# Kernel tuning notes

Measured on AMD Instinct MI355X. Metric: run time of the kernel, lower is better.

The kernel has to match this reference:

```python
import jax, jax.numpy as jnp
import numpy as np

N_TOKENS = 32768
D_MODEL = 1024
NUM_CODES = 4096
CODE_DEPTH = 256


def setup_inputs() -> dict:
    key = jax.random.key(0)
    kx, kc, kw, kb = jax.random.split(key, 4)
    x = jax.random.normal(kx, (N_TOKENS, D_MODEL), dtype=jnp.float32)
    # codebook init mirrors the torch module: randn, row-normalized, first column zeroed
    cb = jax.random.normal(kc, (NUM_CODES, CODE_DEPTH), dtype=jnp.float32)
    cb = cb / jnp.linalg.norm(cb, axis=-1, keepdims=True)
    cb = cb.at[:, 0].set(0.0)
    W_down = jax.random.normal(kw, (D_MODEL, CODE_DEPTH), dtype=jnp.float32) * (D_MODEL ** -0.5)
    b_down = jax.random.normal(kb, (CODE_DEPTH,), dtype=jnp.float32) * 0.01
    return {"x": x, "codebook": cb, "W_down": W_down, "b_down": b_down}


def reference(x, codebook, W_down, b_down):
    # downsample d_model -> code_depth, then L2-normalize (eps=1e-6)
    z = x @ W_down + b_down                                   # [N, D]
    z = z / (jnp.linalg.norm(z, axis=-1, keepdims=True) + 1e-6)
    # squared euclidean distances to codebook[1:] (argmin of sq == argmin of cdist)
    cb = codebook[1:]                                         # [K-1, D]
    sq = (jnp.sum(z * z, axis=-1, keepdims=True)
          - 2.0 * (z @ cb.T)
          + jnp.sum(cb * cb, axis=-1))                        # [N, K-1]
    code_indices = jnp.argmin(sq, axis=-1) + 1                # [N], in [1, K)
    hard_codes = codebook[code_indices]                       # [N, D] gather
    return z, code_indices, hard_codes
```

## Files before the change

### kernel.cpp

```cpp
#include <hip/hip_runtime.h>
#include <math.h>
#include <stdint.h>

#define NT 32768
#define DM 1024
#define NC 4096
#define CD 256

#define X_F4 (DM/4)
#define W_F4 (CD/4)
#define Z_F4 (CD/4)
#define C_F4 (CD/4)

#define CDE 272
#define CDE_B (CDE*2)
#define TILE_B (32*CDE_B)

typedef __attribute__((ext_vector_type(8))) short bf16x8;
typedef __attribute__((ext_vector_type(4))) float floatx4;
typedef __attribute__((ext_vector_type(16))) float floatx16;

__device__ __forceinline__ unsigned short f2bf(float f) {
    union { float f; uint32_t u; } v; v.f = f;
    uint32_t u = v.u;
    u += 0x7FFFu + ((u >> 16) & 1u);
    return (unsigned short)(u >> 16);
}

__device__ __forceinline__ void split8(const float4 f0, const float4 f1,
                                       bf16x8& h, bf16x8& l) {
    float f[8] = {f0.x, f0.y, f0.z, f0.w, f1.x, f1.y, f1.z, f1.w};
    #pragma unroll
    for (int j = 0; j < 8; ++j) {
        union { float f; uint32_t u; } v; v.f = f[j];
        h[j] = (short)(v.u >> 16);
        union { uint32_t u; float f; } t; t.u = v.u & 0xFFFF0000u;
        l[j] = (short)f2bf(f[j] - t.f);
    }
}

__global__ __launch_bounds__(256) void k0_prep(const float4* __restrict__ cb,
                                               ushort* __restrict__ cbb2) {
    int wid = threadIdx.x >> 6, lane = threadIdx.x & 63;
    int code = blockIdx.x * 4 + wid;
    float4 c = cb[(size_t)code * C_F4 + lane];
    ushort4 h;
    h.x = f2bf(c.x); h.y = f2bf(c.y); h.z = f2bf(c.z); h.w = f2bf(c.w);
    *(ushort4*)(cbb2 + (size_t)code * CDE + lane * 4) = h;
    float ss = c.x*c.x + c.y*c.y + c.z*c.z + c.w*c.w;
    #pragma unroll
    for (int m = 32; m >= 1; m >>= 1) ss += __shfl_xor(ss, m, 64);
    if (lane == 0) {
        float nh = 2.0f - 0.5f * ss;
        union { float f; uint32_t u; } v; v.f = nh;
        uint32_t uh = v.u & 0xFFFF0000u;
        union { uint32_t u; float f; } t; t.u = uh;
        ushort* p = cbb2 + (size_t)code * CDE + 256;
        p[0] = (ushort)(uh >> 16);
        p[1] = f2bf(nh - t.f);
        #pragma unroll
        for (int i = 2; i < 16; ++i) p[i] = 0;
    }
}

__global__ __launch_bounds__(256) void k0b_wsplit(const float4* __restrict__ W,
                                                  ushort* __restrict__ WTh,
                                                  ushort* __restrict__ WTl) {
    __shared__ float lds[16][260];
    int slab = blockIdx.x;
    int tid = threadIdx.x;
    #pragma unroll
    for (int jj = 0; jj < 4; ++jj) {
        int v = jj * 256 + tid;
        int row = v >> 6, f4 = v & 63;
        float4 d = W[(size_t)(slab * 16 + row) * W_F4 + f4];
        *(float4*)&lds[row][f4 * 4] = d;
    }
    __syncthreads();
    int c = tid;
    #pragma unroll
    for (int kb = 0; kb < 2; ++kb) {
        bf16x8 h, l;
        #pragma unroll
        for (int j = 0; j < 8; ++j) {
            float x = lds[kb * 8 + j][c];
            union { float f; uint32_t u; } v; v.f = x;
            h[j] = (short)(v.u >> 16);
            union { uint32_t u; float f; } t; t.u = v.u & 0xFFFF0000u;
            l[j] = (short)f2bf(x - t.f);
        }
        size_t off = (size_t)c * 1024 + slab * 16 + kb * 8;
        *(bf16x8*)(WTh + off) = h;
        *(bf16x8*)(WTl + off) = l;
    }
}

__global__ __launch_bounds__(256, 2) void k1_gemm1(const float4* __restrict__ X,
                                                   const ushort* __restrict__ WTh,
                                                   const ushort* __restrict__ WTl,
                                                   float4* __restrict__ Zp) {
    __shared__ __align__(16) char lds[65536];
    char* Ah = lds;
    char* Al = lds + 16384;
    char* Bh = lds + 32768;
    char* Bl = lds + 49152;

    int tid  = threadIdx.x;
    int w    = tid >> 6, lane = tid & 63;
    int wm   = w >> 1, wn = w & 1;
    int c    = lane & 15, q = lane >> 4;
    int mb   = blockIdx.x >> 1, nb = blockIdx.x & 1;
    int m0   = mb * 128;
    int n0   = nb * 128;

    auto issue_loads = [&](int kt, float4* ga, bf16x8* gbh, bf16x8* gbl) {
        #pragma unroll
        for (int jj = 0; jj < 4; ++jj) {
            int v = jj * 256 + tid;
            int row = v >> 3, ch = v & 7;
            const float4* p = X + (size_t)(m0 + row) * X_F4 + kt * 16 + ch * 2;
            ga[jj * 2]     = p[0];
            ga[jj * 2 + 1] = p[1];
        }
        #pragma unroll
        for (int jj = 0; jj < 4; ++jj) {
            int v = jj * 256 + tid;
            int col = v >> 3, ch = v & 7;
            size_t off = (size_t)(n0 + col) * 1024 + kt * 64 + ch * 8;
            gbh[jj] = *(const bf16x8*)(WTh + off);
            gbl[jj] = *(const bf16x8*)(WTl + off);
        }
    };
    auto write_lds = [&](const float4* ga, const bf16x8* gbh, const bf16x8* gbl) {
        #pragma unroll
        for (int jj = 0; jj < 4; ++jj) {
            int v = jj * 256 + tid;
            int row = v >> 3, ch = v & 7;
            bf16x8 h, l;
            split8(ga[jj * 2], ga[jj * 2 + 1], h, l);
            int off = row * 128 + ((ch ^ (row & 7)) << 4);
            *(bf16x8*)(Ah + off) = h;
            *(bf16x8*)(Al + off) = l;
        }
        #pragma unroll
        for (int jj = 0; jj < 4; ++jj) {
            int v = jj * 256 + tid;
            int col = v >> 3, ch = v & 7;
            int off = col * 128 + ((ch ^ (col & 7)) << 4);
            *(bf16x8*)(Bh + off) = gbh[jj];
            *(bf16x8*)(Bl + off) = gbl[jj];
        }
    };

    floatx4 acc[4][4];
    #pragma unroll
    for (int i = 0; i < 4; ++i)
        #pragma unroll
        for (int j = 0; j < 4; ++j) acc[i][j] = (floatx4){0.f, 0.f, 0.f, 0.f};

    float4 ga[8]; bf16x8 gbh[4], gbl[4];
    issue_loads(0, ga, gbh, gbl);
    write_lds(ga, gbh, gbl);

    for (int kt = 0; kt < 16; ++kt) {
        __syncthreads();
        if (kt < 15) issue_loads(kt + 1, ga, gbh, gbl);

        #pragma unroll
        for (int ks = 0; ks < 2; ++ks) {
            bf16x8 xh[4], xl[4], wh[4], wl[4];
            #pragma unroll
            for (int i = 0; i < 4; ++i) {
                int xrow = wm * 64 + i * 16 + c;
                int xoff = xrow * 128 + (((ks * 4 + q) ^ (xrow & 7)) << 4);
                xh[i] = *(const bf16x8*)(Ah + xoff);
                xl[i] = *(const bf16x8*)(Al + xoff);
                int wrow = wn * 64 + i * 16 + c;
                int woff = wrow * 128 + (((ks * 4 + q) ^ (wrow & 7)) << 4);
                wh[i] = *(const bf16x8*)(Bh + woff);
                wl[i] = *(const bf16x8*)(Bl + woff);
            }
            #pragma unroll
            for (int xi = 0; xi < 4; ++xi)
                #pragma unroll
                for (int ni = 0; ni < 4; ++ni) {
                    acc[xi][ni] = __builtin_amdgcn_mfma_f32_16x16x32_bf16(wh[ni], xh[xi], acc[xi][ni], 0, 0, 0);
                    acc[xi][ni] = __builtin_amdgcn_mfma_f32_16x16x32_bf16(wh[ni], xl[xi], acc[xi][ni], 0, 0, 0);
                    acc[xi][ni] = __builtin_amdgcn_mfma_f32_16x16x32_bf16(wl[ni], xh[xi], acc[xi][ni], 0, 0, 0);
                }
        }

        __syncthreads();
        if (kt < 15) write_lds(ga, gbh, gbl);
    }

    #pragma unroll
    for (int xi = 0; xi < 4; ++xi) {
        int tok = m0 + wm * 64 + xi * 16 + c;
        #pragma unroll
        for (int ni = 0; ni < 4; ++ni) {
            int nf4 = nb * 32 + wn * 16 + ni * 4 + q;
            float4 o;
            o.x = acc[xi][ni][0]; o.y = acc[xi][ni][1];
            o.z = acc[xi][ni][2]; o.w = acc[xi][ni][3];
            Zp[(size_t)tok * Z_F4 + nf4] = o;
        }
    }
}

__global__ __launch_bounds__(256) void k1b_norm(float4* __restrict__ Z,
                                                const float4* __restrict__ bias) {
    int wid = threadIdx.x >> 6, lane = threadIdx.x & 63;
    int t = blockIdx.x * 4 + wid;
    float4 b = bias[lane];
    float4 z = Z[(size_t)t * Z_F4 + lane];
    z.x += b.x; z.y += b.y; z.z += b.z; z.w += b.w;
    double ss = (double)z.x*z.x + (double)z.y*z.y + (double)z.z*z.z + (double)z.w*z.w;
    #pragma unroll
    for (int m = 32; m >= 1; m >>= 1) ss += __shfl_xor(ss, m, 64);
    float inv = 1.0f / ((float)sqrt(ss) + 1e-6f);
    z.x *= inv; z.y *= inv; z.z *= inv; z.w *= inv;
    Z[(size_t)t * Z_F4 + lane] = z;
}

__global__ __launch_bounds__(256, 1) void k2_mfma(const float* __restrict__ Z,
                                                  const ushort* __restrict__ Cbb2,
                                                  int4* __restrict__ cands) {
    __shared__ uint32_t Mk[128][2][4];

    int tid  = threadIdx.x;
    int wm   = tid >> 6;
    int lane = tid & 63;
    int r    = lane & 31;
    int hi   = lane >> 5;
    int t0   = blockIdx.x * 128;

    bf16x8 Bt[17];
    #pragma unroll
    for (int f = 0; f < 16; ++f) {
        const float* zp = Z + (size_t)(t0 + wm * 32 + r) * CD + f * 16 + hi * 8;
        float4 f0 = *(const float4*)zp;
        float4 f1 = *(const float4*)(zp + 4);
        bf16x8 b;
        b[0] = (short)f2bf(f0.x); b[1] = (short)f2bf(f0.y);
        b[2] = (short)f2bf(f0.z); b[3] = (short)f2bf(f0.w);
        b[4] = (short)f2bf(f1.x); b[5] = (short)f2bf(f1.y);
        b[6] = (short)f2bf(f1.z); b[7] = (short)f2bf(f1.w);
        Bt[f] = b;
    }
    {
        bf16x8 b = (bf16x8){0, 0, 0, 0, 0, 0, 0, 0};
        if (hi == 0) { b[0] = (short)0x3F80; b[1] = (short)0x3F80; }
        Bt[16] = b;
    }

    int r0 = (r == 0) ? 1 : r;
    const char* abase   = (const char*)Cbb2;
    const char* ap_lane = abase + r * CDE_B + hi * 16;
    const char* ap0     = abase + r0 * CDE_B + hi * 16;

    uint32_t K1v = 0, K2v = 0, K3v = 0, K4v = 0;

    bf16x8 A0[17], A1[17];
    #pragma unroll
    for (int f = 0; f < 17; ++f) A0[f] = *(const bf16x8*)(ap0 + f * 32);

    const char* ap = ap_lane + TILE_B;

    auto compute = [&](const bf16x8 (&Ax)[17], int ct) {
        floatx16 Cc;
        #pragma unroll
        for (int i = 0; i < 16; ++i) Cc[i] = 0.0f;
        #pragma unroll
        for (int f = 0; f < 17; ++f)
            Cc = __builtin_amdgcn_mfma_f32_32x32x16_bf16(Ax[f], Bt[f], Cc, 0, 0, 0);
        #pragma unroll
        for (int reg = 0; reg < 16; ++reg) {
            union { float f; uint32_t u; } uv; uv.f = Cc[reg];
            uint32_t k = (uv.u & 0xFFFFF800u) | ((uint32_t)ct << 4) | (uint32_t)reg;
            uint32_t t;
            t = k < K1v ? k : K1v;  K1v = k > K1v ? k : K1v;  k = t;
            t = k < K2v ? k : K2v;  K2v = k > K2v ? k : K2v;  k = t;
            t = k < K3v ? k : K3v;  K3v = k > K3v ? k : K3v;  k = t;
            K4v = k > K4v ? k : K4v;
        }
    };

    for (int ct = 0; ct < 128; ct += 2) {
        #pragma unroll
        for (int f = 0; f < 17; ++f) A1[f] = *(const bf16x8*)(ap + f * 32);
        ap += TILE_B;
        compute(A0, ct);
        const char* apn = (ct + 2 < 128) ? ap : ap_lane;
        #pragma unroll
        for (int f = 0; f < 17; ++f) A0[f] = *(const bf16x8*)(apn + f * 32);
        ap += TILE_B;
        compute(A1, ct + 1);
        if ((ct & 15) == 14) __builtin_amdgcn_s_barrier();
    }

    int lt = wm * 32 + r;
    Mk[lt][hi][0] = K1v; Mk[lt][hi][1] = K2v;
    Mk[lt][hi][2] = K3v; Mk[lt][hi][3] = K4v;
    __syncthreads();

    if (tid < 128) {
        uint32_t bk0 = 0, bk1 = 0, bk2 = 0, bk3 = 0;
        uint32_t be0 = 0, be1 = 0, be2 = 0, be3 = 0;
        #pragma unroll
        for (int e = 0; e < 8; ++e) {
            uint32_t key = Mk[tid][e >> 2][e & 3];
            if (key > bk0) {
                bk3 = bk2; be3 = be2; bk2 = bk1; be2 = be1;
                bk1 = bk0; be1 = be0; bk0 = key; be0 = (uint32_t)e;
            } else if (key > bk1) {
                bk3 = bk2; be3 = be2; bk2 = bk1; be2 = be1; bk1 = key; be1 = (uint32_t)e;
            } else if (key > bk2) {
                bk3 = bk2; be3 = be2; bk2 = key; be2 = (uint32_t)e;
            } else if (key > bk3) {
                bk3 = key; be3 = (uint32_t)e;
            }
        }
        auto dec = [&](uint32_t key, uint32_t e) -> int {
            int ct = (int)((key >> 4) & 127u);
            int rg = (int)(key & 15u);
            int row = (rg & 3) + 8 * (rg >> 2) + 4 * (int)(e >> 2);
            int code = ct * 32 + row;
            return code < 1 ? 1 : code;
        };
        int4 out;
        out.x = dec(bk0, be0); out.y = dec(bk1, be1);
        out.z = dec(bk2, be2); out.w = dec(bk3, be3);
        cands[t0 + tid] = out;
    }
}

__global__ __launch_bounds__(256) void k3_refine(const float4* __restrict__ Z,
                                                 const float4* __restrict__ Cb,
                                                 const int4* __restrict__ cands,
                                                 float* __restrict__ idxOut,
                                                 float4* __restrict__ hardOut) {
    int wid = threadIdx.x >> 6, lane = threadIdx.x & 63;
    int t = blockIdx.x * 4 + wid;
    int4 cd = cands[t];
    int cc[4] = {cd.x, cd.y, cd.z, cd.w};
    float4 z = Z[(size_t)t * Z_F4 + lane];
    double best = -1.0e300;
    int bi = NC;
    #pragma unroll
    for (int e = 0; e < 4; ++e) {
        int idx = cc[e];
        float4 cf = Cb[(size_t)idx * C_F4 + lane];
        double dot = (double)z.x*cf.x + (double)z.y*cf.y + (double)z.z*cf.z + (double)z.w*cf.w;
        double nrm = (double)cf.x*cf.x + (double)cf.y*cf.y + (double)cf.z*cf.z + (double)cf.w*cf.w;
        #pragma unroll
        for (int m = 32; m >= 1; m >>= 1) {
            dot += __shfl_xor(dot, m, 64);
            nrm += __shfl_xor(nrm, m, 64);
        }
        double s = dot - 0.5 * nrm;
        if (idx >= 1 && (s > best || (s == best && idx < bi))) { best = s; bi = idx; }
    }
    if (lane == 0) idxOut[t] = (float)bi;
    hardOut[(size_t)t * C_F4 + lane] = Cb[(size_t)bi * C_F4 + lane];
}

extern "C" void kernel_launch(void* const* d_in, const int* in_sizes, int n_in,
                              void* d_out, int out_size, void* d_ws, size_t ws_size,
                              hipStream_t stream) {
    const float* x  = (const float*)d_in[0];
    const float* cb = (const float*)d_in[1];
    const float* w  = (const float*)d_in[2];
    const float* bd = (const float*)d_in[3];

    float* zOut    = (float*)d_out;
    float* idxOut  = zOut + (size_t)NT * CD;
    float* hardOut = idxOut + NT;

    int4*   cands = (int4*)d_ws;
    ushort* cbb2  = (ushort*)((char*)d_ws + 524288);
    ushort* wth   = (ushort*)((char*)d_ws + 2752512);
    ushort* wtl   = (ushort*)((char*)d_ws + 3276800);

    k0_prep<<<NC / 4, 256, 0, stream>>>((const float4*)cb, cbb2);
    k0b_wsplit<<<DM / 16, 256, 0, stream>>>((const float4*)w, wth, wtl);
    k1_gemm1<<<(NT / 128) * 2, 256, 0, stream>>>((const float4*)x, wth, wtl,
                                                 (float4*)zOut);
    k1b_norm<<<NT / 4, 256, 0, stream>>>((float4*)zOut, (const float4*)bd);
    k2_mfma<<<NT / 128, 256, 0, stream>>>(zOut, cbb2, cands);
    k3_refine<<<NT / 4, 256, 0, stream>>>((const float4*)zOut, (const float4*)cb,
                                          cands, idxOut, (float4*)hardOut);
}
```

Measured before the change: 441.0 us.

## Tile codebook into MFMA-fragment layout and split codes across waves

```diff
diff --git a/kernel.cpp b/kernel.cpp
--- a/kernel.cpp
+++ b/kernel.cpp
@@ -12,9 +12,7 @@
 #define Z_F4 (CD/4)
 #define C_F4 (CD/4)
 
-#define CDE 272
-#define CDE_B (CDE*2)
-#define TILE_B (32*CDE_B)
+#define TILE_B 17408
 
 typedef __attribute__((ext_vector_type(8))) short bf16x8;
 typedef __attribute__((ext_vector_type(4))) float floatx4;
@@ -41,25 +39,36 @@
 
 __global__ __launch_bounds__(256) void k0_prep(const float4* __restrict__ cb,
                                                ushort* __restrict__ cbb2) {
-    int wid = threadIdx.x >> 6, lane = threadIdx.x & 63;
-    int code = blockIdx.x * 4 + wid;
-    float4 c = cb[(size_t)code * C_F4 + lane];
-    ushort4 h;
-    h.x = f2bf(c.x); h.y = f2bf(c.y); h.z = f2bf(c.z); h.w = f2bf(c.w);
-    *(ushort4*)(cbb2 + (size_t)code * CDE + lane * 4) = h;
-    float ss = c.x*c.x + c.y*c.y + c.z*c.z + c.w*c.w;
-    #pragma unroll
-    for (int m = 32; m >= 1; m >>= 1) ss += __shfl_xor(ss, m, 64);
-    if (lane == 0) {
+    int tid = threadIdx.x;
+    int l = tid & 63, wid = tid >> 6;
+    int code = blockIdx.x * 8 + wid * 2 + (l >> 5);
+    int fr = l & 31, f = fr >> 1, hi = fr & 1;
+    const float4* p = cb + (size_t)code * C_F4 + f * 4 + hi * 2;
+    float4 f0 = p[0], f1 = p[1];
+    bf16x8 h;
+    h[0] = (short)f2bf(f0.x); h[1] = (short)f2bf(f0.y);
+    h[2] = (short)f2bf(f0.z); h[3] = (short)f2bf(f0.w);
+    h[4] = (short)f2bf(f1.x); h[5] = (short)f2bf(f1.y);
+    h[6] = (short)f2bf(f1.z); h[7] = (short)f2bf(f1.w);
+    float ss = f0.x*f0.x + f0.y*f0.y + f0.z*f0.z + f0.w*f0.w
+             + f1.x*f1.x + f1.y*f1.y + f1.z*f1.z + f1.w*f1.w;
+    #pragma unroll
+    for (int m = 16; m >= 1; m >>= 1) ss += __shfl_xor(ss, m, 64);
+    int ct = code >> 5, r = code & 31;
+    char* base = (char*)cbb2 + (size_t)ct * TILE_B;
+    *(bf16x8*)(base + f * 1024 + (((hi << 5) | r) << 4)) = h;
+    if (fr == 0) {
         float nh = 2.0f - 0.5f * ss;
         union { float f; uint32_t u; } v; v.f = nh;
         uint32_t uh = v.u & 0xFFFF0000u;
         union { uint32_t u; float f; } t; t.u = uh;
-        ushort* p = cbb2 + (size_t)code * CDE + 256;
-        p[0] = (ushort)(uh >> 16);
-        p[1] = f2bf(nh - t.f);
-        #pragma unroll
-        for (int i = 2; i < 16; ++i) p[i] = 0;
+        bf16x8 e = (bf16x8){0, 0, 0, 0, 0, 0, 0, 0};
+        e[0] = (short)(uh >> 16);
+        e[1] = (short)f2bf(nh - t.f);
+        *(bf16x8*)(base + 16 * 1024 + (r << 4)) = e;
+    } else if (fr == 1) {
+        bf16x8 z = (bf16x8){0, 0, 0, 0, 0, 0, 0, 0};
+        *(bf16x8*)(base + 16 * 1024 + ((32 | r) << 4)) = z;
     }
 }
 
@@ -223,17 +232,19 @@
     Z[(size_t)t * Z_F4 + lane] = z;
 }
 
-__global__ __launch_bounds__(256, 1) void k2_mfma(const float* __restrict__ Z,
+__global__ __launch_bounds__(256, 2) void k2_mfma(const float* __restrict__ Z,
                                                   const ushort* __restrict__ Cbb2,
                                                   int4* __restrict__ cands) {
-    __shared__ uint32_t Mk[128][2][4];
+    __shared__ uint32_t Mk[64][4][4];
 
     int tid  = threadIdx.x;
-    int wm   = tid >> 6;
+    int w    = tid >> 6;
+    int wm   = w >> 1;
+    int wc   = w & 1;
     int lane = tid & 63;
     int r    = lane & 31;
     int hi   = lane >> 5;
-    int t0   = blockIdx.x * 128;
+    int t0   = blockIdx.x * 64;
 
     bf16x8 Bt[17];
     #pragma unroll
@@ -254,18 +265,18 @@
         Bt[16] = b;
     }
 
-    int r0 = (r == 0) ? 1 : r;
-    const char* abase   = (const char*)Cbb2;
-    const char* ap_lane = abase + r * CDE_B + hi * 16;
-    const char* ap0     = abase + r0 * CDE_B + hi * 16;
-
-    uint32_t K1v = 0, K2v = 0, K3v = 0, K4v = 0;
+    const char* half = (const char*)Cbb2 + (size_t)(wc * 64) * TILE_B;
+    int l0 = (wc == 0 && r == 0) ? (lane + 1) : lane;
+    const char* ap0 = half + l0 * 16;
+    const char* apL = half + lane * 16;
+
+    float K1f = 0.0f, K2f = 0.0f, K3f = 0.0f, K4f = 0.0f;
 
     bf16x8 A0[17], A1[17];
     #pragma unroll
-    for (int f = 0; f < 17; ++f) A0[f] = *(const bf16x8*)(ap0 + f * 32);
-
-    const char* ap = ap_lane + TILE_B;
+    for (int f = 0; f < 17; ++f) A0[f] = *(const bf16x8*)(ap0 + f * 1024);
+
+    const char* ap = apL + TILE_B;
 
     auto compute = [&](const bf16x8 (&Ax)[17], int ct) {
         floatx16 Cc;
@@ -277,54 +288,63 @@
         #pragma unroll
         for (int reg = 0; reg < 16; ++reg) {
             union { float f; uint32_t u; } uv; uv.f = Cc[reg];
-            uint32_t k = (uv.u & 0xFFFFF800u) | ((uint32_t)ct << 4) | (uint32_t)reg;
-            uint32_t t;
-            t = k < K1v ? k : K1v;  K1v = k > K1v ? k : K1v;  k = t;
-            t = k < K2v ? k : K2v;  K2v = k > K2v ? k : K2v;  k = t;
-            t = k < K3v ? k : K3v;  K3v = k > K3v ? k : K3v;  k = t;
-            K4v = k > K4v ? k : K4v;
+            uint32_t ku = (uv.u & 0xFFFFF800u) | ((uint32_t)ct << 4) | (uint32_t)reg;
+            union { uint32_t u; float f; } kv; kv.u = ku;
+            float k = kv.f;
+            K4f = __builtin_amdgcn_fmed3f(K3f, K4f, k);
+            K3f = __builtin_amdgcn_fmed3f(K2f, K3f, k);
+            K2f = __builtin_amdgcn_fmed3f(K1f, K2f, k);
+            K1f = fmaxf(K1f, k);
         }
     };
 
-    for (int ct = 0; ct < 128; ct += 2) {
-        #pragma unroll
-        for (int f = 0; f < 17; ++f) A1[f] = *(const bf16x8*)(ap + f * 32);
+    for (int ctl = 0; ctl < 64; ctl += 2) {
+        #pragma unroll
+        for (int f = 0; f < 17; ++f) A1[f] = *(const bf16x8*)(ap + f * 1024);
         ap += TILE_B;
-        compute(A0, ct);
-        const char* apn = (ct + 2 < 128) ? ap : ap_lane;
-        #pragma unroll
-        for (int f = 0; f < 17; ++f) A0[f] = *(const bf16x8*)(apn + f * 32);
+        compute(A0, wc * 64 + ctl);
+        const char* apn = (ctl + 2 < 64) ? ap : apL;
+        #pragma unroll
+        for (int f = 0; f < 17; ++f) A0[f] = *(const bf16x8*)(apn + f * 1024);
         ap += TILE_B;
-        compute(A1, ct + 1);
-        if ((ct & 15) == 14) __builtin_amdgcn_s_barrier();
-    }
-
-    int lt = wm * 32 + r;
-    Mk[lt][hi][0] = K1v; Mk[lt][hi][1] = K2v;
-    Mk[lt][hi][2] = K3v; Mk[lt][hi][3] = K4v;
+        compute(A1, wc * 64 + ctl + 1);
+        if ((ctl & 15) == 14) __builtin_amdgcn_s_barrier();
+    }
+
+    {
+        int lt = wm * 32 + r, src = wc * 2 + hi;
+        union { float f; uint32_t u; } a, b, c, d;
+        a.f = K1f; b.f = K2f; c.f = K3f; d.f = K4f;
+        Mk[lt][src][0] = a.u; Mk[lt][src][1] = b.u;
+        Mk[lt][src][2] = c.u; Mk[lt][src][3] = d.u;
+    }
     __syncthreads();
 
-    if (tid < 128) {
+    if (tid < 64) {
         uint32_t bk0 = 0, bk1 = 0, bk2 = 0, bk3 = 0;
         uint32_t be0 = 0, be1 = 0, be2 = 0, be3 = 0;
         #pragma unroll
-        for (int e = 0; e < 8; ++e) {
-            uint32_t key = Mk[tid][e >> 2][e & 3];
-            if (key > bk0) {
-                bk3 = bk2; be3 = be2; bk2 = bk1; be2 = be1;
-                bk1 = bk0; be1 = be0; bk0 = key; be0 = (uint32_t)e;
-            } else if (key > bk1) {
-                bk3 = bk2; be3 = be2; bk2 = bk1; be2 = be1; bk1 = key; be1 = (uint32_t)e;
-            } else if (key > bk2) {
-                bk3 = bk2; be3 = be2; bk2 = key; be2 = (uint32_t)e;
-            } else if (key > bk3) {
-                bk3 = key; be3 = (uint32_t)e;
+        for (int s = 0; s < 4; ++s) {
+            #pragma unroll
+            for (int j = 0; j < 4; ++j) {
+                uint32_t key = Mk[tid][s][j];
+                uint32_t e = (uint32_t)s;
+                if (key > bk0) {
+                    bk3 = bk2; be3 = be2; bk2 = bk1; be2 = be1;
+                    bk1 = bk0; be1 = be0; bk0 = key; be0 = e;
+                } else if (key > bk1) {
+                    bk3 = bk2; be3 = be2; bk2 = bk1; be2 = be1; bk1 = key; be1 = e;
+                } else if (key > bk2) {
+                    bk3 = bk2; be3 = be2; bk2 = key; be2 = e;
+                } else if (key > bk3) {
+                    bk3 = key; be3 = e;
+                }
             }
         }
         auto dec = [&](uint32_t key, uint32_t e) -> int {
             int ct = (int)((key >> 4) & 127u);
             int rg = (int)(key & 15u);
-            int row = (rg & 3) + 8 * (rg >> 2) + 4 * (int)(e >> 2);
+            int row = (rg & 3) + 8 * (rg >> 2) + 4 * (int)(e & 1);
             int code = ct * 32 + row;
             return code < 1 ? 1 : code;
         };
@@ -382,12 +402,12 @@
     ushort* wth   = (ushort*)((char*)d_ws + 2752512);
     ushort* wtl   = (ushort*)((char*)d_ws + 3276800);
 
-    k0_prep<<<NC / 4, 256, 0, stream>>>((const float4*)cb, cbb2);
+    k0_prep<<<NC / 8, 256, 0, stream>>>((const float4*)cb, cbb2);
     k0b_wsplit<<<DM / 16, 256, 0, stream>>>((const float4*)w, wth, wtl);
     k1_gemm1<<<(NT / 128) * 2, 256, 0, stream>>>((const float4*)x, wth, wtl,
                                                  (float4*)zOut);
     k1b_norm<<<NT / 4, 256, 0, stream>>>((float4*)zOut, (const float4*)bd);
-    k2_mfma<<<NT / 128, 256, 0, stream>>>(zOut, cbb2, cands);
+    k2_mfma<<<NT / 64, 256, 0, stream>>>(zOut, cbb2, cands);
     k3_refine<<<NT / 4, 256, 0, stream>>>((const float4*)zOut, (const float4*)cb,
                                           cands, idxOut, (float4*)hardOut);
 }
```

Result: faster. 392.2 us (-11.1%).
